# Performance work log

Measured on AMD Instinct MI355X. Metric: run time of the kernel, lower is better.

The kernel has to match this reference:

```python
import jax, jax.numpy as jnp
import numpy as np

H = 1024

def _lstm_layer(xs, h, c, W_ih, W_hh, b):
    # xs: [B, T, H]; precompute input projections as one big GEMM
    gx = jnp.einsum('bth,gh->btg', xs, W_ih) + b  # [B, T, 4H]
    gx = jnp.swapaxes(gx, 0, 1)  # [T, B, 4H]

    def step(carry, g_t):
        h, c = carry
        g = g_t + h @ W_hh.T  # [B, 4H]
        i, f, gg, o = jnp.split(g, 4, axis=-1)  # PyTorch gate order i,f,g,o
        c = jax.nn.sigmoid(f) * c + jax.nn.sigmoid(i) * jnp.tanh(gg)
        h = jax.nn.sigmoid(o) * jnp.tanh(c)
        return (h, c), h

    (h, c), ys = jax.lax.scan(step, (h, c), gx)
    return jnp.swapaxes(ys, 0, 1), h, c  # [B, T, H]


def setup_inputs() -> dict:
    key = jax.random.key(0)
    ks = jax.random.split(key, 12)
    B, T, V = 64, 256, 128
    std = 1.0 / np.sqrt(H)

    def xavier(k, shape):
        fan_in, fan_out = shape[1], shape[0]
        lim = np.sqrt(6.0 / (fan_in + fan_out))
        return jax.random.uniform(k, shape, jnp.float32, -lim, lim)

    return {
        'x': jax.random.randint(ks[0], (B, T), 0, V),
        'emb': jax.random.normal(ks[1], (V, H), jnp.float32),
        'W_ih0': xavier(ks[2], (4 * H, H)),
        'W_hh0': jax.random.normal(ks[3], (4 * H, H), jnp.float32) * std,
        'b0': jnp.zeros((4 * H,), jnp.float32).at[H:2 * H].set(2.0),
        'W_ih1': xavier(ks[4], (4 * H, H)),
        'W_hh1': jax.random.normal(ks[5], (4 * H, H), jnp.float32) * std,
        'b1': jnp.zeros((4 * H,), jnp.float32).at[H:2 * H].set(2.0),
        'fc_W': jax.random.normal(ks[6], (V, H), jnp.float32) * np.sqrt(2.0 / (V + H)),
        'fc_b': jnp.zeros((V,), jnp.float32),
        'h0': jax.random.normal(ks[7], (2, B, H), jnp.float32) * std,
        'c0': jax.random.normal(ks[8], (2, B, H), jnp.float32) * std,
    }


def reference(x, emb, W_ih0, W_hh0, b0, W_ih1, W_hh1, b1, fc_W, fc_b, h0, c0):
    embedded = emb[x]  # [B, T, H]
    y0, _, _ = _lstm_layer(embedded, h0[0], c0[0], W_ih0, W_hh0, b0)
    # dropout between layers and after lstm is identity in eval mode
    y1, _, _ = _lstm_layer(y0, h0[1], c0[1], W_ih1, W_hh1, b1)
    return jnp.einsum('bth,vh->btv', y1, fc_W) + fc_b  # [B, T, V]
```

## Files before the change

### kernel.cpp

```cpp
#include <hip/hip_runtime.h>

#define HD 1024
#define BB 64
#define TT 256
#define VV 128
#define NSTEPS (TT + 3)
#define KSTR 1056
#define HS (BB * KSTR)
#define GXS (4 * HD * BB)
#define NBLKW 388
#define GRID (NBLKW + 1)
#define GO_OFF 7936
#define CHUNK 32768
#define LDS_BYTES (65536 + 8192)

typedef __attribute__((ext_vector_type(8))) short bf16x8;
typedef __attribute__((ext_vector_type(4))) float f32x4;

#define MFMA16(a, b, c) __builtin_amdgcn_mfma_f32_16x16x32_bf16((a), (b), (c), 0, 0, 0)

__device__ __forceinline__ unsigned short f2bf(float f) {
  union { float f; unsigned u; } v; v.f = f;
  unsigned r = v.u + 0x7fffu + ((v.u >> 16) & 1u);
  return (unsigned short)(r >> 16);
}
__device__ __forceinline__ float bf2f(unsigned short h) {
  union { unsigned u; float f; } v; v.u = ((unsigned)h) << 16; return v.f;
}
__device__ __forceinline__ float sigf(float x) { return 1.0f / (1.0f + __expf(-x)); }
__device__ __forceinline__ float tanh_f(float x) { return 1.0f - 2.0f / (__expf(2.0f * x) + 1.0f); }

__global__ __launch_bounds__(256) void init_misc(
    const int* __restrict__ x, const float* __restrict__ emb,
    const float* __restrict__ h0in, const float* __restrict__ c0in,
    int* __restrict__ xT, float* __restrict__ embT,
    unsigned short* __restrict__ h0bh, unsigned short* __restrict__ h0bl,
    unsigned short* __restrict__ h1bh, unsigned short* __restrict__ h1bl,
    float* __restrict__ c0, float* __restrict__ c1,
    int* __restrict__ bar)
{
  int tid = blockIdx.x * blockDim.x + threadIdx.x;
  int stride = gridDim.x * blockDim.x;
  const int nXT = TT * BB, nE = VV * HD, nS = HD * BB, nB = 8192;
  const int total = nXT + nE + 4 * nS + nB;
  for (int i = tid; i < total; i += stride) {
    int j = i;
    if (j < nXT) { xT[j] = x[(j & 63) * TT + (j >> 6)]; continue; }
    j -= nXT;
    if (j < nE) { embT[j] = emb[(j & 127) * HD + (j >> 7)]; continue; }
    j -= nE;
    if (j < nS) { int b = j >> 10, n = j & 1023;
      float v = h0in[b * HD + n];
      unsigned short hi = f2bf(v);
      h0bh[HS + b * KSTR + n] = hi;
      h0bl[HS + b * KSTR + n] = f2bf(v - bf2f(hi));
      continue; }
    j -= nS;
    if (j < nS) { int b = j >> 10, n = j & 1023;
      float v = h0in[nS + b * HD + n];
      unsigned short hi = f2bf(v);
      h1bh[HS + b * KSTR + n] = hi;
      h1bl[HS + b * KSTR + n] = f2bf(v - bf2f(hi));
      continue; }
    j -= nS;
    if (j < nS) { int n = j >> 6, b = j & 63;
      c0[n * BB + b] = c0in[b * HD + n]; continue; }
    j -= nS;
    if (j < nS) { int n = j >> 6, b = j & 63;
      c1[n * BB + b] = c0in[nS + b * HD + n]; continue; }
    j -= nS;
    bar[j] = 0;
  }
}

__global__ __launch_bounds__(256) void embproj_kernel(
    const float* __restrict__ Wih0, const float* __restrict__ b0,
    const float* __restrict__ embT, float* __restrict__ embprojT)
{
  const int lane = threadIdx.x & 63;
  const int wave = (blockIdx.x * blockDim.x + threadIdx.x) >> 6;
  const int n0 = __builtin_amdgcn_readfirstlane(wave * 4);
  const float* __restrict__ r0 = Wih0 + (size_t)n0 * HD;
  const float* __restrict__ r1 = r0 + HD;
  const float* __restrict__ r2 = r1 + HD;
  const float* __restrict__ r3 = r2 + HD;
  float a00=0,a01=0,a10=0,a11=0,a20=0,a21=0,a30=0,a31=0;
  #pragma unroll 4
  for (int k = 0; k < HD; ++k) {
    float e0 = embT[k * VV + lane];
    float e1 = embT[k * VV + 64 + lane];
    float w0 = r0[k], w1 = r1[k], w2 = r2[k], w3 = r3[k];
    a00 = fmaf(e0, w0, a00); a01 = fmaf(e1, w0, a01);
    a10 = fmaf(e0, w1, a10); a11 = fmaf(e1, w1, a11);
    a20 = fmaf(e0, w2, a20); a21 = fmaf(e1, w2, a21);
    a30 = fmaf(e0, w3, a30); a31 = fmaf(e1, w3, a31);
  }
  float bb0 = b0[n0], bb1 = b0[n0+1], bb2 = b0[n0+2], bb3 = b0[n0+3];
  embprojT[(n0+0)*VV + lane]      = a00 + bb0;
  embprojT[(n0+0)*VV + 64 + lane] = a01 + bb0;
  embprojT[(n0+1)*VV + lane]      = a10 + bb1;
  embprojT[(n0+1)*VV + 64 + lane] = a11 + bb1;
  embprojT[(n0+2)*VV + lane]      = a20 + bb2;
  embprojT[(n0+2)*VV + 64 + lane] = a21 + bb2;
  embprojT[(n0+3)*VV + lane]      = a30 + bb3;
  embprojT[(n0+3)*VV + 64 + lane] = a31 + bb3;
}

__global__ __launch_bounds__(256) void swizzle_kernel(
    const float* __restrict__ Whh0, const float* __restrict__ Wih1,
    const float* __restrict__ Whh1, const float* __restrict__ fcW,
    unsigned short* __restrict__ wzh, unsigned short* __restrict__ wzl)
{
  int W = (blockIdx.x * blockDim.x + threadIdx.x) >> 6;
  int lane = threadIdx.x & 63;
  int blk = W >> 6, rem = W & 63;
  int mt = rem >> 5, kt = rem & 31;
  int m = lane & 15, q = lane >> 4;
  int rho = mt * 16 + m;
  const float* src; int srow;
  if (blk < 128)      { src = Whh0; srow = (rho >> 3) * HD + blk * 8 + (rho & 7); }
  else if (blk < 256) { src = Wih1; srow = (blk - 128) * 32 + rho; }
  else if (blk < 384) { src = Whh1; srow = (rho >> 3) * HD + (blk - 256) * 8 + (rho & 7); }
  else                { src = fcW;  srow = (blk - 384) * 32 + rho; }
  int k0 = kt * 32 + q * 8;
  const float* sp = src + (size_t)srow * HD + k0;
  uint4 ohi, olo;
  unsigned short* ph = (unsigned short*)&ohi;
  unsigned short* pl = (unsigned short*)&olo;
  #pragma unroll
  for (int j = 0; j < 8; ++j) {
    float wv = sp[j];
    unsigned short hi = f2bf(wv);
    ph[j] = hi;
    pl[j] = f2bf(wv - bf2f(hi));
  }
  size_t off = (size_t)blk * CHUNK + ((size_t)(mt * 32 + kt) * 64 + lane) * 8;
  *(uint4*)(wzh + off) = ohi;
  *(uint4*)(wzl + off) = olo;
}

__global__ __launch_bounds__(128) void scan_kernel(
    const unsigned short* __restrict__ wzh,
    const unsigned short* __restrict__ wzl,
    const float* __restrict__ embprojT,
    const int* __restrict__ xT,
    unsigned short* __restrict__ h0bh, unsigned short* __restrict__ h0bl,
    unsigned short* __restrict__ h1bh, unsigned short* __restrict__ h1bl,
    float* __restrict__ c0,
    float* __restrict__ c1,
    float* __restrict__ gx1,
    const float* __restrict__ b1v,
    const float* __restrict__ fcb,
    float* __restrict__ out,
    int* __restrict__ bar)
{
  extern __shared__ char smem[];
  const bf16x8* wfrag = (const bf16x8*)smem;
  float* red = (float*)(smem + 65536);

  const int tid = threadIdx.x, lane = tid & 63, w = tid >> 6;
  const int blk = blockIdx.x;

  if (blk == NBLKW) {
    const int f0 = tid, f1 = tid + 128, f2 = tid + 256;
    for (int s = 1; s <= NSTEPS; ++s) {
      while (__hip_atomic_load(&bar[f0 * 16], __ATOMIC_RELAXED, __HIP_MEMORY_SCOPE_AGENT) < s)
        __builtin_amdgcn_s_sleep(1);
      while (__hip_atomic_load(&bar[f1 * 16], __ATOMIC_RELAXED, __HIP_MEMORY_SCOPE_AGENT) < s)
        __builtin_amdgcn_s_sleep(1);
      while (__hip_atomic_load(&bar[f2 * 16], __ATOMIC_RELAXED, __HIP_MEMORY_SCOPE_AGENT) < s)
        __builtin_amdgcn_s_sleep(1);
      if (tid < 4)
        while (__hip_atomic_load(&bar[(384 + tid) * 16], __ATOMIC_RELAXED, __HIP_MEMORY_SCOPE_AGENT) < s)
          __builtin_amdgcn_s_sleep(1);
      __syncthreads();
      if (tid == 0) {
        __builtin_amdgcn_fence(__ATOMIC_ACQUIRE, "agent");
        __hip_atomic_store(&bar[GO_OFF], s, __ATOMIC_RELAXED, __HIP_MEMORY_SCOPE_AGENT);
      }
    }
    return;
  }

  {
    const uint4* srcp = (const uint4*)(wzh + (size_t)blk * CHUNK);
    uint4* dst = (uint4*)smem;
    for (int i = tid; i < 4096; i += 128) dst[i] = srcp[i];
  }
  __syncthreads();
  const unsigned short* wlo = wzl + (size_t)blk * CHUNK;

  int part, n0 = 0, rg0 = 0;
  if (blk < 128)      { part = 0; n0 = blk * 8; }
  else if (blk < 256) { part = 1; rg0 = (blk - 128) * 32; }
  else if (blk < 384) { part = 2; n0 = (blk - 256) * 8; }
  else                { part = 3; rg0 = (blk - 384) * 32; }

  int goff0 = (0 * 16 + (lane & 15)) * KSTR + (lane >> 4) * 8;
  int goff1 = (1 * 16 + (lane & 15)) * KSTR + (lane >> 4) * 8;
  int goff2 = (2 * 16 + (lane & 15)) * KSTR + (lane >> 4) * 8;
  int goff3 = (3 * 16 + (lane & 15)) * KSTR + (lane >> 4) * 8;
  const int kt0 = w * 16;

  for (int s = 0; s < NSTEPS; ++s) {
    bool active = (part == 0) ? (s < TT)
                : (part == 1) ? (s >= 1 && s <= TT)
                : (part == 2) ? (s >= 2 && s <= TT + 1)
                :               (s >= 3);
    if (active) {
      const int ps = (s + 1) & 1, cs2 = s & 1;
      const bool l0src = (part == 0 || part == 1);
      const unsigned short* hsrcH = (l0src ? h0bh : h1bh) + ps * HS;
      const unsigned short* hsrcL = (l0src ? h0bl : h1bl) + ps * HS;
      const unsigned short* hbh0 = hsrcH + goff0;
      const unsigned short* hbh1 = hsrcH + goff1;
      const unsigned short* hbh2 = hsrcH + goff2;
      const unsigned short* hbh3 = hsrcH + goff3;
      const unsigned short* hbl0 = hsrcL + goff0;
      const unsigned short* hbl1 = hsrcL + goff1;
      const unsigned short* hbl2 = hsrcL + goff2;
      const unsigned short* hbl3 = hsrcL + goff3;

      f32x4 acc[2][4];
      #pragma unroll
      for (int i = 0; i < 2; ++i)
        #pragma unroll
        for (int j = 0; j < 4; ++j) acc[i][j] = (f32x4){0.f, 0.f, 0.f, 0.f};

      #pragma unroll 4
      for (int kk = 0; kk < 16; ++kk) {
        int kt = kt0 + kk;
        bf16x8 a0  = wfrag[kt * 64 + lane];
        bf16x8 a1  = wfrag[(32 + kt) * 64 + lane];
        bf16x8 a0l = *(const bf16x8*)(wlo + ((size_t)(0 * 32 + kt) * 64 + lane) * 8);
        bf16x8 a1l = *(const bf16x8*)(wlo + ((size_t)(1 * 32 + kt) * 64 + lane) * 8);
        bf16x8 b0  = *(const bf16x8*)(hbh0 + kt * 32);
        bf16x8 b1  = *(const bf16x8*)(hbh1 + kt * 32);
        bf16x8 b2  = *(const bf16x8*)(hbh2 + kt * 32);
        bf16x8 b3  = *(const bf16x8*)(hbh3 + kt * 32);
        bf16x8 c0f = *(const bf16x8*)(hbl0 + kt * 32);
        bf16x8 c1f = *(const bf16x8*)(hbl1 + kt * 32);
        bf16x8 c2f = *(const bf16x8*)(hbl2 + kt * 32);
        bf16x8 c3f = *(const bf16x8*)(hbl3 + kt * 32);
        acc[0][0] = MFMA16(a0, b0, acc[0][0]);
        acc[0][1] = MFMA16(a0, b1, acc[0][1]);
        acc[0][2] = MFMA16(a0, b2, acc[0][2]);
        acc[0][3] = MFMA16(a0, b3, acc[0][3]);
        acc[1][0] = MFMA16(a1, b0, acc[1][0]);
        acc[1][1] = MFMA16(a1, b1, acc[1][1]);
        acc[1][2] = MFMA16(a1, b2, acc[1][2]);
        acc[1][3] = MFMA16(a1, b3, acc[1][3]);
        acc[0][0] = MFMA16(a0, c0f, acc[0][0]);
        acc[0][1] = MFMA16(a0, c1f, acc[0][1]);
        acc[0][2] = MFMA16(a0, c2f, acc[0][2]);
        acc[0][3] = MFMA16(a0, c3f, acc[0][3]);
        acc[1][0] = MFMA16(a1, c0f, acc[1][0]);
        acc[1][1] = MFMA16(a1, c1f, acc[1][1]);
        acc[1][2] = MFMA16(a1, c2f, acc[1][2]);
        acc[1][3] = MFMA16(a1, c3f, acc[1][3]);
        acc[0][0] = MFMA16(a0l, b0, acc[0][0]);
        acc[0][1] = MFMA16(a0l, b1, acc[0][1]);
        acc[0][2] = MFMA16(a0l, b2, acc[0][2]);
        acc[0][3] = MFMA16(a0l, b3, acc[0][3]);
        acc[1][0] = MFMA16(a1l, b0, acc[1][0]);
        acc[1][1] = MFMA16(a1l, b1, acc[1][1]);
        acc[1][2] = MFMA16(a1l, b2, acc[1][2]);
        acc[1][3] = MFMA16(a1l, b3, acc[1][3]);
      }

      #pragma unroll
      for (int ro = 0; ro < 2; ++ro) {
        #pragma unroll
        for (int mt = 0; mt < 2; ++mt)
          #pragma unroll
          for (int ntl = 0; ntl < 2; ++ntl) {
            f32x4 v = acc[mt][ro * 2 + ntl];
            int base = w * 1024 + (mt * 16 + (lane >> 4) * 4) * 32 + ntl * 16 + (lane & 15);
            red[base + 0 * 32] = v[0];
            red[base + 1 * 32] = v[1];
            red[base + 2 * 32] = v[2];
            red[base + 3 * 32] = v[3];
          }
        __syncthreads();

        if (part == 0 || part == 2) {
          int nl = tid >> 4, bp = (tid & 15) * 2;
          int b = ro * 32 + bp;
          int n = n0 + nl;
          float2 p0, p1, p2, p3;
          {
            int ix = (0 * 8 + nl) * 32 + bp;
            float2 u0 = *(const float2*)&red[ix], u1 = *(const float2*)&red[1024 + ix];
            p0 = make_float2(u0.x + u1.x, u0.y + u1.y);
            ix = (1 * 8 + nl) * 32 + bp;
            u0 = *(const float2*)&red[ix]; u1 = *(const float2*)&red[1024 + ix];
            p1 = make_float2(u0.x + u1.x, u0.y + u1.y);
            ix = (2 * 8 + nl) * 32 + bp;
            u0 = *(const float2*)&red[ix]; u1 = *(const float2*)&red[1024 + ix];
            p2 = make_float2(u0.x + u1.x, u0.y + u1.y);
            ix = (3 * 8 + nl) * 32 + bp;
            u0 = *(const float2*)&red[ix]; u1 = *(const float2*)&red[1024 + ix];
            p3 = make_float2(u0.x + u1.x, u0.y + u1.y);
          }
          float pi0, pf0, pg0, po0, pi1, pf1, pg1, po1;
          if (part == 0) {
            int xv0 = xT[s * BB + b], xv1 = xT[s * BB + b + 1];
            pi0 = p0.x + embprojT[(0 * HD + n) * VV + xv0];
            pf0 = p1.x + embprojT[(1 * HD + n) * VV + xv0];
            pg0 = p2.x + embprojT[(2 * HD + n) * VV + xv0];
            po0 = p3.x + embprojT[(3 * HD + n) * VV + xv0];
            pi1 = p0.y + embprojT[(0 * HD + n) * VV + xv1];
            pf1 = p1.y + embprojT[(1 * HD + n) * VV + xv1];
            pg1 = p2.y + embprojT[(2 * HD + n) * VV + xv1];
            po1 = p3.y + embprojT[(3 * HD + n) * VV + xv1];
          } else {
            const float* gx = gx1 + ps * GXS;
            float2 q0 = *(const float2*)&gx[(0 * HD + n) * BB + b];
            float2 q1 = *(const float2*)&gx[(1 * HD + n) * BB + b];
            float2 q2 = *(const float2*)&gx[(2 * HD + n) * BB + b];
            float2 q3 = *(const float2*)&gx[(3 * HD + n) * BB + b];
            pi0 = p0.x + q0.x; pf0 = p1.x + q1.x; pg0 = p2.x + q2.x; po0 = p3.x + q3.x;
            pi1 = p0.y + q0.y; pf1 = p1.y + q1.y; pg1 = p2.y + q2.y; po1 = p3.y + q3.y;
          }
          float* cc = (part == 0) ? c0 : c1;
          float2 cold = *(const float2*)&cc[n * BB + b];
          float cn0 = sigf(pf0) * cold.x + sigf(pi0) * tanh_f(pg0);
          float cn1 = sigf(pf1) * cold.y + sigf(pi1) * tanh_f(pg1);
          *(float2*)&cc[n * BB + b] = make_float2(cn0, cn1);
          float hv0 = sigf(po0) * tanh_f(cn0);
          float hv1 = sigf(po1) * tanh_f(cn1);
          unsigned short* hwh = ((part == 0) ? h0bh : h1bh) + cs2 * HS;
          unsigned short* hwl = ((part == 0) ? h0bl : h1bl) + cs2 * HS;
          unsigned short e0 = f2bf(hv0);
          unsigned short e1 = f2bf(hv1);
          hwh[b * KSTR + n]       = e0;
          hwh[(b + 1) * KSTR + n] = e1;
          hwl[b * KSTR + n]       = f2bf(hv0 - bf2f(e0));
          hwl[(b + 1) * KSTR + n] = f2bf(hv1 - bf2f(e1));
        } else {
          int rb = (tid >> 4) * 4, bp = (tid & 15) * 2;
          int b = ro * 32 + bp;
          #pragma unroll
          for (int rr = 0; rr < 4; ++rr) {
            int rho = rb + rr, ix = rho * 32 + bp;
            float2 u0 = *(const float2*)&red[ix], u1 = *(const float2*)&red[1024 + ix];
            if (part == 1) {
              float bias = b1v[rg0 + rho];
              float2 sm = make_float2(u0.x + u1.x + bias, u0.y + u1.y + bias);
              *(float2*)&gx1[cs2 * GXS + (rg0 + rho) * BB + b] = sm;
            } else {
              float bias = fcb[rg0 + rho];
              int t = s - 3;
              out[(size_t)b * (TT * VV) + t * VV + rg0 + rho]       = u0.x + u1.x + bias;
              out[(size_t)(b + 1) * (TT * VV) + t * VV + rg0 + rho] = u0.y + u1.y + bias;
            }
          }
        }
        __syncthreads();
      }
    }

    if (tid == 0) {
      __builtin_amdgcn_fence(__ATOMIC_RELEASE, "agent");
      __hip_atomic_store(&bar[blk * 16], s + 1, __ATOMIC_RELAXED, __HIP_MEMORY_SCOPE_AGENT);
      while (__hip_atomic_load(&bar[GO_OFF], __ATOMIC_RELAXED, __HIP_MEMORY_SCOPE_AGENT) < s + 1)
        __builtin_amdgcn_s_sleep(1);
      __builtin_amdgcn_fence(__ATOMIC_ACQUIRE, "agent");
    }
    __syncthreads();
  }
}

extern "C" void kernel_launch(void* const* d_in, const int* in_sizes, int n_in,
                              void* d_out, int out_size, void* d_ws, size_t ws_size,
                              hipStream_t stream) {
  (void)in_sizes; (void)n_in; (void)out_size; (void)ws_size;
  const int*   x    = (const int*)d_in[0];
  const float* emb  = (const float*)d_in[1];
  const float* Wih0 = (const float*)d_in[2];
  const float* Whh0 = (const float*)d_in[3];
  const float* b0   = (const float*)d_in[4];
  const float* Wih1 = (const float*)d_in[5];
  const float* Whh1 = (const float*)d_in[6];
  const float* b1   = (const float*)d_in[7];
  const float* fcW  = (const float*)d_in[8];
  const float* fcb  = (const float*)d_in[9];
  const float* h0in = (const float*)d_in[10];
  const float* c0in = (const float*)d_in[11];
  float* out = (float*)d_out;
  char* ws = (char*)d_ws;

  unsigned short* wzh      = (unsigned short*)(ws + 0);
  unsigned short* wzl      = (unsigned short*)(ws + 25427968);
  float*          embprojT = (float*)(ws + 50855936);
  float*          embT     = (float*)(ws + 52953088);
  unsigned short* h0bh     = (unsigned short*)(ws + 53477376);
  unsigned short* h0bl     = (unsigned short*)(ws + 53747712);
  unsigned short* h1bh     = (unsigned short*)(ws + 54018048);
  unsigned short* h1bl     = (unsigned short*)(ws + 54288384);
  float*          c0       = (float*)(ws + 54558720);
  float*          c1       = (float*)(ws + 54820864);
  float*          gx1      = (float*)(ws + 55083008);
  int*            xT       = (int*)(ws + 57180160);
  int*            bar      = (int*)(ws + 57245696);

  hipLaunchKernelGGL(init_misc, dim3(512), dim3(256), 0, stream,
                     x, emb, h0in, c0in, xT, embT, h0bh, h0bl, h1bh, h1bl, c0, c1, bar);
  hipLaunchKernelGGL(swizzle_kernel, dim3(6208), dim3(256), 0, stream,
                     Whh0, Wih1, Whh1, fcW, wzh, wzl);
  hipLaunchKernelGGL(embproj_kernel, dim3(256), dim3(256), 0, stream,
                     Wih0, b0, embT, embprojT);

  hipFuncSetAttribute((const void*)scan_kernel,
                      hipFuncAttributeMaxDynamicSharedMemorySize, LDS_BYTES);

  void* args[] = {
    (void*)&wzh, (void*)&wzl, (void*)&embprojT, (void*)&xT,
    (void*)&h0bh, (void*)&h0bl, (void*)&h1bh, (void*)&h1bl,
    (void*)&c0, (void*)&c1, (void*)&gx1, (void*)&b1, (void*)&fcb, (void*)&out,
    (void*)&bar
  };
  hipLaunchCooperativeKernel((void*)scan_kernel, dim3(GRID), dim3(128),
                             args, LDS_BYTES, stream);
}
```

Before: 7.714 ms.

## Replace coordinator-block barrier with decentralized flag polling and register-cache low weights

Drops the dedicated coordinator block that gathered all per-block flags and published a single go flag. Each worker block now polls every block's flag itself, which removes one hop of global-memory latency from each of the roughly 260 step barriers. The trade-off is many more polling loads hitting the same flag lines. The low-half bf16 weight fragments are also loaded once into registers instead of being re-read from global memory every step, at the cost of much higher register pressure.

```diff
diff --git a/kernel.cpp b/kernel.cpp
--- a/kernel.cpp
+++ b/kernel.cpp
@@ -9,8 +9,6 @@
 #define HS (BB * KSTR)
 #define GXS (4 * HD * BB)
 #define NBLKW 388
-#define GRID (NBLKW + 1)
-#define GO_OFF 7936
 #define CHUNK 32768
 #define LDS_BYTES (65536 + 8192)
 
@@ -139,7 +137,7 @@
   *(uint4*)(wzl + off) = olo;
 }
 
-__global__ __launch_bounds__(128) void scan_kernel(
+__global__ __launch_bounds__(128, 2) void scan_kernel(
     const unsigned short* __restrict__ wzh,
     const unsigned short* __restrict__ wzl,
     const float* __restrict__ embprojT,
@@ -160,35 +158,23 @@
 
   const int tid = threadIdx.x, lane = tid & 63, w = tid >> 6;
   const int blk = blockIdx.x;
-
-  if (blk == NBLKW) {
-    const int f0 = tid, f1 = tid + 128, f2 = tid + 256;
-    for (int s = 1; s <= NSTEPS; ++s) {
-      while (__hip_atomic_load(&bar[f0 * 16], __ATOMIC_RELAXED, __HIP_MEMORY_SCOPE_AGENT) < s)
-        __builtin_amdgcn_s_sleep(1);
-      while (__hip_atomic_load(&bar[f1 * 16], __ATOMIC_RELAXED, __HIP_MEMORY_SCOPE_AGENT) < s)
-        __builtin_amdgcn_s_sleep(1);
-      while (__hip_atomic_load(&bar[f2 * 16], __ATOMIC_RELAXED, __HIP_MEMORY_SCOPE_AGENT) < s)
-        __builtin_amdgcn_s_sleep(1);
-      if (tid < 4)
-        while (__hip_atomic_load(&bar[(384 + tid) * 16], __ATOMIC_RELAXED, __HIP_MEMORY_SCOPE_AGENT) < s)
-          __builtin_amdgcn_s_sleep(1);
-      __syncthreads();
-      if (tid == 0) {
-        __builtin_amdgcn_fence(__ATOMIC_ACQUIRE, "agent");
-        __hip_atomic_store(&bar[GO_OFF], s, __ATOMIC_RELAXED, __HIP_MEMORY_SCOPE_AGENT);
-      }
-    }
-    return;
-  }
+  const int kt0 = w * 16;
 
   {
     const uint4* srcp = (const uint4*)(wzh + (size_t)blk * CHUNK);
     uint4* dst = (uint4*)smem;
     for (int i = tid; i < 4096; i += 128) dst[i] = srcp[i];
   }
+  bf16x8 lo0[16], lo1[16];
+  {
+    const unsigned short* wlo = wzl + (size_t)blk * CHUNK;
+    #pragma unroll
+    for (int kk = 0; kk < 16; ++kk) {
+      lo0[kk] = *(const bf16x8*)(wlo + ((size_t)(0 * 32 + kt0 + kk) * 64 + lane) * 8);
+      lo1[kk] = *(const bf16x8*)(wlo + ((size_t)(1 * 32 + kt0 + kk) * 64 + lane) * 8);
+    }
+  }
   __syncthreads();
-  const unsigned short* wlo = wzl + (size_t)blk * CHUNK;
 
   int part, n0 = 0, rg0 = 0;
   if (blk < 128)      { part = 0; n0 = blk * 8; }
@@ -200,7 +186,6 @@
   int goff1 = (1 * 16 + (lane & 15)) * KSTR + (lane >> 4) * 8;
   int goff2 = (2 * 16 + (lane & 15)) * KSTR + (lane >> 4) * 8;
   int goff3 = (3 * 16 + (lane & 15)) * KSTR + (lane >> 4) * 8;
-  const int kt0 = w * 16;
 
   for (int s = 0; s < NSTEPS; ++s) {
     bool active = (part == 0) ? (s < TT)
@@ -232,8 +217,6 @@
         int kt = kt0 + kk;
         bf16x8 a0  = wfrag[kt * 64 + lane];
         bf16x8 a1  = wfrag[(32 + kt) * 64 + lane];
-        bf16x8 a0l = *(const bf16x8*)(wlo + ((size_t)(0 * 32 + kt) * 64 + lane) * 8);
-        bf16x8 a1l = *(const bf16x8*)(wlo + ((size_t)(1 * 32 + kt) * 64 + lane) * 8);
         bf16x8 b0  = *(const bf16x8*)(hbh0 + kt * 32);
         bf16x8 b1  = *(const bf16x8*)(hbh1 + kt * 32);
         bf16x8 b2  = *(const bf16x8*)(hbh2 + kt * 32);
@@ -258,14 +241,14 @@
         acc[1][1] = MFMA16(a1, c1f, acc[1][1]);
         acc[1][2] = MFMA16(a1, c2f, acc[1][2]);
         acc[1][3] = MFMA16(a1, c3f, acc[1][3]);
-        acc[0][0] = MFMA16(a0l, b0, acc[0][0]);
-        acc[0][1] = MFMA16(a0l, b1, acc[0][1]);
-        acc[0][2] = MFMA16(a0l, b2, acc[0][2]);
-        acc[0][3] = MFMA16(a0l, b3, acc[0][3]);
-        acc[1][0] = MFMA16(a1l, b0, acc[1][0]);
-        acc[1][1] = MFMA16(a1l, b1, acc[1][1]);
-        acc[1][2] = MFMA16(a1l, b2, acc[1][2]);
-        acc[1][3] = MFMA16(a1l, b3, acc[1][3]);
+        acc[0][0] = MFMA16(lo0[kk], b0, acc[0][0]);
+        acc[0][1] = MFMA16(lo0[kk], b1, acc[0][1]);
+        acc[0][2] = MFMA16(lo0[kk], b2, acc[0][2]);
+        acc[0][3] = MFMA16(lo0[kk], b3, acc[0][3]);
+        acc[1][0] = MFMA16(lo1[kk], b0, acc[1][0]);
+        acc[1][1] = MFMA16(lo1[kk], b1, acc[1][1]);
+        acc[1][2] = MFMA16(lo1[kk], b2, acc[1][2]);
+        acc[1][3] = MFMA16(lo1[kk], b3, acc[1][3]);
       }
 
       #pragma unroll
@@ -360,14 +343,20 @@
       }
     }
 
+    __syncthreads();
     if (tid == 0) {
       __builtin_amdgcn_fence(__ATOMIC_RELEASE, "agent");
       __hip_atomic_store(&bar[blk * 16], s + 1, __ATOMIC_RELAXED, __HIP_MEMORY_SCOPE_AGENT);
-      while (__hip_atomic_load(&bar[GO_OFF], __ATOMIC_RELAXED, __HIP_MEMORY_SCOPE_AGENT) < s + 1)
+    }
+    while (__hip_atomic_load(&bar[tid * 16], __ATOMIC_RELAXED, __HIP_MEMORY_SCOPE_AGENT) < s + 1)
+      __builtin_amdgcn_s_sleep(1);
+    while (__hip_atomic_load(&bar[(128 + tid) * 16], __ATOMIC_RELAXED, __HIP_MEMORY_SCOPE_AGENT) < s + 1)
+      __builtin_amdgcn_s_sleep(1);
+    if (256 + tid < NBLKW)
+      while (__hip_atomic_load(&bar[(256 + tid) * 16], __ATOMIC_RELAXED, __HIP_MEMORY_SCOPE_AGENT) < s + 1)
         __builtin_amdgcn_s_sleep(1);
-      __builtin_amdgcn_fence(__ATOMIC_ACQUIRE, "agent");
-    }
     __syncthreads();
+    __builtin_amdgcn_fence(__ATOMIC_ACQUIRE, "agent");
   }
 }
 
@@ -420,6 +409,6 @@
     (void*)&c0, (void*)&c1, (void*)&gx1, (void*)&b1, (void*)&fcb, (void*)&out,
     (void*)&bar
   };
-  hipLaunchCooperativeKernel((void*)scan_kernel, dim3(GRID), dim3(128),
+  hipLaunchCooperativeKernel((void*)scan_kernel, dim3(NBLKW), dim3(128),
                              args, LDS_BYTES, stream);
 }
```

After: 9.809 ms. 1.27x slower.

## Replace barrier fences with agent-scope atomic loads/stores and keep cell state in registers

Applied to the files above, without the earlier changes.

Removes the agent-scope release/acquire fences around the per-step grid barrier. Cross-block data (h buffers, gx1) is now read and written with relaxed agent-scope atomic loads and stores, so it stays coherent without cache flush or invalidate. The barrier waits on outstanding memory operations and syncs the block before signalling. The LSTM cell state now lives in registers for the whole scan instead of being reloaded and stored in global memory each step, and the launch bounds request two blocks per CU. Correctness depends on the relaxed ordering being enough on this hardware. Splitting the 16-byte loads into 8-byte atomics may add instructions.

```diff
diff --git a/kernel.cpp b/kernel.cpp
--- a/kernel.cpp
+++ b/kernel.cpp
@@ -16,6 +16,7 @@
 
 typedef __attribute__((ext_vector_type(8))) short bf16x8;
 typedef __attribute__((ext_vector_type(4))) float f32x4;
+typedef unsigned long long u64;
 
 #define MFMA16(a, b, c) __builtin_amdgcn_mfma_f32_16x16x32_bf16((a), (b), (c), 0, 0, 0)
 
@@ -29,6 +30,26 @@
 }
 __device__ __forceinline__ float sigf(float x) { return 1.0f / (1.0f + __expf(-x)); }
 __device__ __forceinline__ float tanh_f(float x) { return 1.0f - 2.0f / (__expf(2.0f * x) + 1.0f); }
+
+__device__ __forceinline__ bf16x8 ld_sc16(const unsigned short* p) {
+  union { bf16x8 v; u64 q[2]; } u;
+  const u64* pp = (const u64*)p;
+  u.q[0] = __hip_atomic_load(pp,     __ATOMIC_RELAXED, __HIP_MEMORY_SCOPE_AGENT);
+  u.q[1] = __hip_atomic_load(pp + 1, __ATOMIC_RELAXED, __HIP_MEMORY_SCOPE_AGENT);
+  return u.v;
+}
+__device__ __forceinline__ float2 ld_sc8f(const float* p) {
+  union { float2 f; u64 q; } u;
+  u.q = __hip_atomic_load((const u64*)p, __ATOMIC_RELAXED, __HIP_MEMORY_SCOPE_AGENT);
+  return u.f;
+}
+__device__ __forceinline__ void st_sc8f(float* p, float2 v) {
+  union { float2 f; u64 q; } u; u.f = v;
+  __hip_atomic_store((u64*)p, u.q, __ATOMIC_RELAXED, __HIP_MEMORY_SCOPE_AGENT);
+}
+__device__ __forceinline__ void st_sc2(unsigned short* p, unsigned short v) {
+  __hip_atomic_store(p, v, __ATOMIC_RELAXED, __HIP_MEMORY_SCOPE_AGENT);
+}
 
 __global__ __launch_bounds__(256) void init_misc(
     const int* __restrict__ x, const float* __restrict__ emb,
@@ -139,7 +160,7 @@
   *(uint4*)(wzl + off) = olo;
 }
 
-__global__ __launch_bounds__(128) void scan_kernel(
+__global__ __launch_bounds__(128, 2) void scan_kernel(
     const unsigned short* __restrict__ wzh,
     const unsigned short* __restrict__ wzl,
     const float* __restrict__ embprojT,
@@ -175,12 +196,14 @@
           __builtin_amdgcn_s_sleep(1);
       __syncthreads();
       if (tid == 0) {
-        __builtin_amdgcn_fence(__ATOMIC_ACQUIRE, "agent");
+        asm volatile("" ::: "memory");
         __hip_atomic_store(&bar[GO_OFF], s, __ATOMIC_RELAXED, __HIP_MEMORY_SCOPE_AGENT);
       }
     }
     return;
   }
+
+  const int kt0 = w * 16;
 
   {
     const uint4* srcp = (const uint4*)(wzh + (size_t)blk * CHUNK);
@@ -196,11 +219,21 @@
   else if (blk < 384) { part = 2; n0 = (blk - 256) * 8; }
   else                { part = 3; rg0 = (blk - 384) * 32; }
 
+  float creg[2][2];
+  if (part == 0 || part == 2) {
+    const float* cc = (part == 0) ? c0 : c1;
+    int nl = tid >> 4, bp = (tid & 15) * 2;
+    int n = n0 + nl;
+    float2 v0 = *(const float2*)&cc[n * BB + bp];
+    float2 v1 = *(const float2*)&cc[n * BB + 32 + bp];
+    creg[0][0] = v0.x; creg[0][1] = v0.y;
+    creg[1][0] = v1.x; creg[1][1] = v1.y;
+  }
+
   int goff0 = (0 * 16 + (lane & 15)) * KSTR + (lane >> 4) * 8;
   int goff1 = (1 * 16 + (lane & 15)) * KSTR + (lane >> 4) * 8;
   int goff2 = (2 * 16 + (lane & 15)) * KSTR + (lane >> 4) * 8;
   int goff3 = (3 * 16 + (lane & 15)) * KSTR + (lane >> 4) * 8;
-  const int kt0 = w * 16;
 
   for (int s = 0; s < NSTEPS; ++s) {
     bool active = (part == 0) ? (s < TT)
@@ -234,14 +267,14 @@
         bf16x8 a1  = wfrag[(32 + kt) * 64 + lane];
         bf16x8 a0l = *(const bf16x8*)(wlo + ((size_t)(0 * 32 + kt) * 64 + lane) * 8);
         bf16x8 a1l = *(const bf16x8*)(wlo + ((size_t)(1 * 32 + kt) * 64 + lane) * 8);
-        bf16x8 b0  = *(const bf16x8*)(hbh0 + kt * 32);
-        bf16x8 b1  = *(const bf16x8*)(hbh1 + kt * 32);
-        bf16x8 b2  = *(const bf16x8*)(hbh2 + kt * 32);
-        bf16x8 b3  = *(const bf16x8*)(hbh3 + kt * 32);
-        bf16x8 c0f = *(const bf16x8*)(hbl0 + kt * 32);
-        bf16x8 c1f = *(const bf16x8*)(hbl1 + kt * 32);
-        bf16x8 c2f = *(const bf16x8*)(hbl2 + kt * 32);
-        bf16x8 c3f = *(const bf16x8*)(hbl3 + kt * 32);
+        bf16x8 b0  = ld_sc16(hbh0 + kt * 32);
+        bf16x8 b1  = ld_sc16(hbh1 + kt * 32);
+        bf16x8 b2  = ld_sc16(hbh2 + kt * 32);
+        bf16x8 b3  = ld_sc16(hbh3 + kt * 32);
+        bf16x8 c0f = ld_sc16(hbl0 + kt * 32);
+        bf16x8 c1f = ld_sc16(hbl1 + kt * 32);
+        bf16x8 c2f = ld_sc16(hbl2 + kt * 32);
+        bf16x8 c3f = ld_sc16(hbl3 + kt * 32);
         acc[0][0] = MFMA16(a0, b0, acc[0][0]);
         acc[0][1] = MFMA16(a0, b1, acc[0][1]);
         acc[0][2] = MFMA16(a0, b2, acc[0][2]);
@@ -315,28 +348,26 @@
             po1 = p3.y + embprojT[(3 * HD + n) * VV + xv1];
           } else {
             const float* gx = gx1 + ps * GXS;
-            float2 q0 = *(const float2*)&gx[(0 * HD + n) * BB + b];
-            float2 q1 = *(const float2*)&gx[(1 * HD + n) * BB + b];
-            float2 q2 = *(const float2*)&gx[(2 * HD + n) * BB + b];
-            float2 q3 = *(const float2*)&gx[(3 * HD + n) * BB + b];
+            float2 q0 = ld_sc8f(&gx[(0 * HD + n) * BB + b]);
+            float2 q1 = ld_sc8f(&gx[(1 * HD + n) * BB + b]);
+            float2 q2 = ld_sc8f(&gx[(2 * HD + n) * BB + b]);
+            float2 q3 = ld_sc8f(&gx[(3 * HD + n) * BB + b]);
             pi0 = p0.x + q0.x; pf0 = p1.x + q1.x; pg0 = p2.x + q2.x; po0 = p3.x + q3.x;
             pi1 = p0.y + q0.y; pf1 = p1.y + q1.y; pg1 = p2.y + q2.y; po1 = p3.y + q3.y;
           }
-          float* cc = (part == 0) ? c0 : c1;
-          float2 cold = *(const float2*)&cc[n * BB + b];
-          float cn0 = sigf(pf0) * cold.x + sigf(pi0) * tanh_f(pg0);
-          float cn1 = sigf(pf1) * cold.y + sigf(pi1) * tanh_f(pg1);
-          *(float2*)&cc[n * BB + b] = make_float2(cn0, cn1);
+          float cn0 = sigf(pf0) * creg[ro][0] + sigf(pi0) * tanh_f(pg0);
+          float cn1 = sigf(pf1) * creg[ro][1] + sigf(pi1) * tanh_f(pg1);
+          creg[ro][0] = cn0; creg[ro][1] = cn1;
           float hv0 = sigf(po0) * tanh_f(cn0);
           float hv1 = sigf(po1) * tanh_f(cn1);
           unsigned short* hwh = ((part == 0) ? h0bh : h1bh) + cs2 * HS;
           unsigned short* hwl = ((part == 0) ? h0bl : h1bl) + cs2 * HS;
           unsigned short e0 = f2bf(hv0);
           unsigned short e1 = f2bf(hv1);
-          hwh[b * KSTR + n]       = e0;
-          hwh[(b + 1) * KSTR + n] = e1;
-          hwl[b * KSTR + n]       = f2bf(hv0 - bf2f(e0));
-          hwl[(b + 1) * KSTR + n] = f2bf(hv1 - bf2f(e1));
+          st_sc2(&hwh[b * KSTR + n],       e0);
+          st_sc2(&hwh[(b + 1) * KSTR + n], e1);
+          st_sc2(&hwl[b * KSTR + n],       f2bf(hv0 - bf2f(e0)));
+          st_sc2(&hwl[(b + 1) * KSTR + n], f2bf(hv1 - bf2f(e1)));
         } else {
           int rb = (tid >> 4) * 4, bp = (tid & 15) * 2;
           int b = ro * 32 + bp;
@@ -347,7 +378,7 @@
             if (part == 1) {
               float bias = b1v[rg0 + rho];
               float2 sm = make_float2(u0.x + u1.x + bias, u0.y + u1.y + bias);
-              *(float2*)&gx1[cs2 * GXS + (rg0 + rho) * BB + b] = sm;
+              st_sc8f(&gx1[cs2 * GXS + (rg0 + rho) * BB + b], sm);
             } else {
               float bias = fcb[rg0 + rho];
               int t = s - 3;
@@ -360,14 +391,15 @@
       }
     }
 
+    __builtin_amdgcn_s_waitcnt(0);
+    __syncthreads();
     if (tid == 0) {
-      __builtin_amdgcn_fence(__ATOMIC_RELEASE, "agent");
       __hip_atomic_store(&bar[blk * 16], s + 1, __ATOMIC_RELAXED, __HIP_MEMORY_SCOPE_AGENT);
       while (__hip_atomic_load(&bar[GO_OFF], __ATOMIC_RELAXED, __HIP_MEMORY_SCOPE_AGENT) < s + 1)
         __builtin_amdgcn_s_sleep(1);
-      __builtin_amdgcn_fence(__ATOMIC_ACQUIRE, "agent");
     }
     __syncthreads();
+    asm volatile("" ::: "memory");
   }
 }
 
```

Measured after the change: 6.914 ms. 1.12x faster.
